# Performance work log

Hardware: AMD Instinct MI355X
Metric: run time of the kernel (lower is better)

## Reference

```python
import jax, jax.numpy as jnp
import numpy as np

B, N, H, NH, DEG, NREL = 4, 2048, 768, 12, 16, 64
HD = H // NH          # 64
E = B * N * DEG       # 131072 edges


def setup_inputs() -> dict:
    key = jax.random.key(0)
    ks = jax.random.split(key, 12)
    node_states = jax.random.normal(ks[0], (B, N, H), jnp.float32)

    # Structured edge list so every (batch, dst) pair has DEG distinct src
    # neighbors (unique+coalesce-stable, matching the coalesced sparse tensor).
    b = np.repeat(np.arange(B), N * DEG)
    dst = np.tile(np.repeat(np.arange(N), DEG), B)
    stride = N // DEG
    src = (dst + np.tile(np.arange(DEG), B * N) * stride) % N
    rel = np.random.default_rng(0).integers(0, NREL, size=E)
    edge_indices = jnp.asarray(np.stack([b, dst, src, rel]), jnp.int32)  # (4, E)

    s = 0.02
    Wq = s * jax.random.normal(ks[1], (H, H), jnp.float32)
    bq = s * jax.random.normal(ks[2], (H,), jnp.float32)
    Wk = s * jax.random.normal(ks[3], (H, H), jnp.float32)
    bk = s * jax.random.normal(ks[4], (H,), jnp.float32)
    Wv = s * jax.random.normal(ks[5], (H, H), jnp.float32)
    bv = s * jax.random.normal(ks[6], (H,), jnp.float32)
    # relation embedding tables; row 0 = TOKEN_TO_TOKEN_RELATION_ID zeroed
    Ek = (s * jax.random.normal(ks[7], (NREL, H), jnp.float32)).at[0].set(0.0)
    Ev = (s * jax.random.normal(ks[8], (NREL, H), jnp.float32)).at[0].set(0.0)
    return {"node_states": node_states, "edge_indices": edge_indices,
            "Wq": Wq, "bq": bq, "Wk": Wk, "bk": bk, "Wv": Wv, "bv": bv,
            "Ek": Ek, "Ev": Ev}


def reference(node_states, edge_indices, Wq, bq, Wk, bk, Wv, bv, Ek, Ev):
    Bsz, n_nodes, hidden = node_states.shape
    bi, dst, src, rel = edge_indices

    # dense projections (torch Linear: x @ W.T + b)
    Q = node_states @ Wq.T + bq
    K = node_states @ Wk.T + bk
    V = node_states @ Wv.T + bv

    def heads(x):  # (E, H) -> (E, NH, HD)
        return x.reshape(x.shape[0], NH, HD)

    Qe = heads(Q[bi, dst])     # query gathered at destination node
    Kn = heads(K[bi, src])     # key gathered at source node
    Vn = heads(V[bi, src])
    Ke = heads(Ek[rel])        # edge (relation) key embedding
    Ve = heads(Ev[rel])        # edge (relation) value embedding

    scale = jnp.sqrt(jnp.float32(HD))
    logits = (jnp.sum(Qe * Kn, -1) + jnp.sum(Qe * Ke, -1)) / scale  # (E, NH)

    # sparse softmax over src neighbors per (batch, dst) segment
    seg = bi * n_nodes + dst
    nseg = Bsz * n_nodes
    m = jax.ops.segment_max(logits, seg, num_segments=nseg)
    ex = jnp.exp(logits - m[seg])
    denom = jax.ops.segment_sum(ex, seg, num_segments=nseg)
    attn = ex / denom[seg]                                           # (E, NH)

    # weighted scatter-sum of (node value + edge value) back to dst nodes
    out_e = (attn[..., None] * (Vn + Ve)).reshape(-1, hidden)        # (E, H)
    out = jax.ops.segment_sum(out_e, seg, num_segments=nseg)
    return out.reshape(Bsz, n_nodes, hidden)
```

## Files before the change

kernel.cpp:

```cpp
#include <hip/hip_runtime.h>
#include <hip/hip_bf16.h>

#define BSZ 4
#define NN 2048
#define HH 768
#define NOUT 2304
#define NHEAD 12
#define HD 64
#define DEG 16
#define NREL 64
#define MTOT (BSZ * NN)
#define ETOT (MTOT * DEG)
#define QPAD 776

typedef __attribute__((ext_vector_type(4))) float f32x4;
typedef __attribute__((ext_vector_type(8))) short bf16x8;

__device__ __forceinline__ unsigned short f2bf(float f) {
    union { float f; unsigned int u; } v; v.f = f;
    unsigned int r = v.u + 0x7FFFu + ((v.u >> 16) & 1u);
    return (unsigned short)(r >> 16);
}
__device__ __forceinline__ float bf2f(unsigned short u) {
    union { unsigned int u; float f; } v; v.u = ((unsigned int)u) << 16;
    return v.f;
}

__device__ __forceinline__ void gload16(const unsigned short* g, unsigned short* l) {
    __builtin_amdgcn_global_load_lds(
        (const __attribute__((address_space(1))) unsigned int*)g,
        (__attribute__((address_space(3))) unsigned int*)l,
        16, 0, 0);
}

__global__ __launch_bounds__(256) void convert_all(
    const float* __restrict__ X,
    const float* __restrict__ Wq, const float* __restrict__ Wk,
    const float* __restrict__ Wv,
    const float* __restrict__ bq, const float* __restrict__ bk,
    const float* __restrict__ bv,
    const float* __restrict__ Ek, const float* __restrict__ Ev,
    unsigned short* __restrict__ Xb, unsigned short* __restrict__ Wb,
    float* __restrict__ biasb,
    unsigned short* __restrict__ Ekb, unsigned short* __restrict__ Evb)
{
    const int blk = blockIdx.x;
    if (blk < 3072) {
        const size_t i = ((size_t)blk * 256 + threadIdx.x) * 8;
        const float4 a = *(const float4*)(X + i);
        const float4 b = *(const float4*)(X + i + 4);
        bf16x8 o;
        o[0] = f2bf(a.x); o[1] = f2bf(a.y); o[2] = f2bf(a.z); o[3] = f2bf(a.w);
        o[4] = f2bf(b.x); o[5] = f2bf(b.y); o[6] = f2bf(b.z); o[7] = f2bf(b.w);
        *(bf16x8*)(Xb + i) = o;
    } else if (blk < 3936) {
        const int tid = (blk - 3072) * 256 + threadIdx.x;
        const size_t i = (size_t)tid * 8;
        const int row = (int)(i / HH);
        const size_t off = i - (size_t)row * HH;
        const float* src = (row < HH) ? (Wq + (size_t)row * HH)
                         : (row < 2 * HH) ? (Wk + (size_t)(row - HH) * HH)
                                          : (Wv + (size_t)(row - 2 * HH) * HH);
        const float4 a = *(const float4*)(src + off);
        const float4 b = *(const float4*)(src + off + 4);
        bf16x8 o;
        o[0] = f2bf(a.x); o[1] = f2bf(a.y); o[2] = f2bf(a.z); o[3] = f2bf(a.w);
        o[4] = f2bf(b.x); o[5] = f2bf(b.y); o[6] = f2bf(b.z); o[7] = f2bf(b.w);
        *(bf16x8*)(Wb + i) = o;
        if (tid < NOUT) {
            biasb[tid] = (tid < HH) ? bq[tid]
                       : (tid < 2 * HH) ? bk[tid - HH] : bv[tid - 2 * HH];
        }
    } else {
        const int blk2 = blk - 3936;
        const int h2 = blk2 / 24;
        const int b2 = blk2 % 24;
        const float* src = h2 ? Ev : Ek;
        unsigned short* dst = h2 ? Evb : Ekb;
        const size_t i = ((size_t)b2 * 256 + threadIdx.x) * 8;
        const float4 a = *(const float4*)(src + i);
        const float4 b = *(const float4*)(src + i + 4);
        bf16x8 o;
        o[0] = f2bf(a.x); o[1] = f2bf(a.y); o[2] = f2bf(a.z); o[3] = f2bf(a.w);
        o[4] = f2bf(b.x); o[5] = f2bf(b.y); o[6] = f2bf(b.z); o[7] = f2bf(b.w);
        *(bf16x8*)(dst + i) = o;
    }
}

__global__ __launch_bounds__(512) void qkv_mfma(
    const unsigned short* __restrict__ Xb,
    const unsigned short* __restrict__ Wb,
    const float* __restrict__ biasb,
    unsigned short* __restrict__ Qb,
    unsigned short* __restrict__ Kb, unsigned short* __restrict__ Vb)
{
    __shared__ unsigned short As0[256 * 32], As1[256 * 32];
    __shared__ unsigned short Bs0[128 * 32], Bs1[128 * 32];

    const int t    = threadIdx.x;
    const int lane = t & 63;
    const int w    = t >> 6;
    const int wr   = w >> 1;
    const int wc   = w & 1;

    const int bid = blockIdx.y * 18 + blockIdx.x;
    const int swz = (bid & 7) * 72 + (bid >> 3);
    const int bn  = (swz % 18) * 128;
    const int bm  = (swz / 18) * 256;

    const int srow  = w * 16 + (lane >> 2);
    const int sslot = ((lane & 3) ^ ((lane >> 2) & 3)) * 8;

    const unsigned short* Asrc0 = Xb + (size_t)(bm + srow) * HH + sslot;
    const unsigned short* Asrc1 = Xb + (size_t)(bm + 128 + srow) * HH + sslot;
    const unsigned short* Bsrc  = Wb + (size_t)(bn + srow) * HH + sslot;

    const int dstoff0 = w * 64 * 8;
    const int dstoff1 = (512 + w * 64) * 8;

    f32x4 acc[4][4];
    #pragma unroll
    for (int ni = 0; ni < 4; ++ni)
        #pragma unroll
        for (int mi = 0; mi < 4; ++mi)
            acc[ni][mi] = (f32x4){0.f, 0.f, 0.f, 0.f};

    const int fr  = lane & 15;
    const int fkp = (((lane >> 4) ^ (lane & 3))) * 8;

#define STAGE(AS, BS, K0) do {                 \
    gload16(Asrc0 + (K0), (AS) + dstoff0);     \
    gload16(Asrc1 + (K0), (AS) + dstoff1);     \
    gload16(Bsrc  + (K0), (BS) + dstoff0);     \
} while (0)

#define COMPUTE(AS, BS) do {                                                  \
    bf16x8 a_[4], b_[4];                                                      \
    _Pragma("unroll")                                                         \
    for (int mi = 0; mi < 4; ++mi)                                            \
        a_[mi] = *(const bf16x8*)((AS) + (wr * 64 + mi * 16 + fr) * 32 + fkp);\
    _Pragma("unroll")                                                         \
    for (int ni = 0; ni < 4; ++ni)                                            \
        b_[ni] = *(const bf16x8*)((BS) + (wc * 64 + ni * 16 + fr) * 32 + fkp);\
    _Pragma("unroll")                                                         \
    for (int ni = 0; ni < 4; ++ni)                                            \
        _Pragma("unroll")                                                     \
        for (int mi = 0; mi < 4; ++mi)                                        \
            acc[ni][mi] = __builtin_amdgcn_mfma_f32_16x16x32_bf16(            \
                b_[ni], a_[mi], acc[ni][mi], 0, 0, 0);                        \
} while (0)

#define WAITV3  asm volatile("s_waitcnt vmcnt(3)" ::: "memory")
#define WAITV0  asm volatile("s_waitcnt vmcnt(0)" ::: "memory")
#define BAR     do { __builtin_amdgcn_s_barrier();                  \
                     asm volatile("" ::: "memory"); } while (0)

    STAGE(As0, Bs0, 0);
    STAGE(As1, Bs1, 32);

    for (int kt = 0; kt < 22; kt += 2) {
        WAITV3; BAR;
        COMPUTE(As0, Bs0);
        BAR;
        STAGE(As0, Bs0, (kt + 2) * 32);
        WAITV3; BAR;
        COMPUTE(As1, Bs1);
        BAR;
        STAGE(As1, Bs1, (kt + 3) * 32);
    }
    WAITV3; BAR;
    COMPUTE(As0, Bs0);
    WAITV0; BAR;
    COMPUTE(As1, Bs1);
#undef STAGE
#undef COMPUTE
#undef WAITV3
#undef WAITV0
#undef BAR

    const int cm = lane & 15;
    const int cn = (lane >> 4) * 4;

    unsigned short* outb; int ncol0;
    if (bn < HH)          { outb = Qb; ncol0 = bn; }
    else if (bn < 2 * HH) { outb = Kb; ncol0 = bn - HH; }
    else                  { outb = Vb; ncol0 = bn - 2 * HH; }

    #pragma unroll
    for (int ni = 0; ni < 4; ++ni) {
        const int nloc = wc * 64 + ni * 16 + cn;
        const float4 b4 = *(const float4*)(biasb + bn + nloc);
        #pragma unroll
        for (int mi = 0; mi < 4; ++mi) {
            const int grow = bm + wr * 64 + mi * 16 + cm;
            ushort4 o;
            o.x = f2bf(acc[ni][mi][0] + b4.x);
            o.y = f2bf(acc[ni][mi][1] + b4.y);
            o.z = f2bf(acc[ni][mi][2] + b4.z);
            o.w = f2bf(acc[ni][mi][3] + b4.w);
            *(ushort4*)(outb + (size_t)grow * HH + ncol0 + nloc) = o;
        }
    }
}

__global__ __launch_bounds__(256) void s2_kernel(
    const unsigned short* __restrict__ Qb,
    const unsigned short* __restrict__ Ekb,
    unsigned short* __restrict__ S2b)
{
    const int t    = threadIdx.x;
    const int lane = t & 63;
    const int w    = t >> 6;
    const int h    = blockIdx.y;
    const int m0   = blockIdx.x * 64 + w * 16;

    const int fr  = lane & 15;
    const int fk8 = (lane >> 4) * 8;

    bf16x8 a[2];
    #pragma unroll
    for (int kk = 0; kk < 2; ++kk)
        a[kk] = *(const bf16x8*)(Qb + (size_t)(m0 + fr) * HH + h * HD + kk * 32 + fk8);

    #pragma unroll
    for (int rt = 0; rt < 4; ++rt) {
        f32x4 acc = (f32x4){0.f, 0.f, 0.f, 0.f};
        #pragma unroll
        for (int kk = 0; kk < 2; ++kk) {
            const bf16x8 bfr = *(const bf16x8*)(
                Ekb + (size_t)(rt * 16 + fr) * HH + h * HD + kk * 32 + fk8);
            acc = __builtin_amdgcn_mfma_f32_16x16x32_bf16(bfr, a[kk], acc, 0, 0, 0);
        }
        const int m   = m0 + (lane & 15);
        const int rel = rt * 16 + (lane >> 4) * 4;
        ushort4 o;
        o.x = f2bf(acc[0]); o.y = f2bf(acc[1]);
        o.z = f2bf(acc[2]); o.w = f2bf(acc[3]);
        *(ushort4*)(S2b + (size_t)m * HH + h * HD + rel) = o;
    }
}

__global__ __launch_bounds__(512) void attn_class(
    const unsigned short* __restrict__ Qb, const unsigned short* __restrict__ Kb,
    const unsigned short* __restrict__ Vb,
    const unsigned short* __restrict__ S2b, const unsigned short* __restrict__ Evb,
    const int* __restrict__ eidx, float* __restrict__ out)
{
    const int bc = blockIdx.x;
    const int b  = bc >> 7;
    const int r  = bc & 127;
    const int t  = threadIdx.x;
    const int lane = t & 63;
    const int w    = t >> 6;

    __shared__ unsigned short s_V[16][QPAD];
    __shared__ float s_attn[16][NHEAD][16];
    __shared__ int s_relslot[16][16];

    if (t < 256) {
        const int j = t >> 4, d = t & 15;
        const size_t e = ((size_t)(b * NN + r + j * 128)) * DEG + d;
        const int src = eidx[2 * ETOT + e];
        const int rel = eidx[3 * ETOT + e];
        const int slot = ((src - r) >> 7) & 15;
        s_relslot[j][slot] = rel;
    }
    for (int g = t; g < 1536; g += 512) {
        const int row = g / 96;
        const int off = (g - row * 96) * 8;
        *(bf16x8*)&s_V[row][off] =
            *(const bf16x8*)(Vb + (size_t)(b * NN + r + row * 128) * HH + off);
    }
    __syncthreads();

    {
        const int fr  = lane & 15;
        const int ig  = lane >> 4;
        const int fk8 = ig * 8;
        const size_t rowb = (size_t)(b * NN + r + fr * 128) * HH;
        #pragma unroll
        for (int hh = 0; hh < 2; ++hh) {
            if (hh == 1 && w >= 4) continue;
            const int h = (hh == 0) ? w : 8 + w;
            f32x4 acc = (f32x4){0.f, 0.f, 0.f, 0.f};
            #pragma unroll
            for (int kk = 0; kk < 2; ++kk) {
                const bf16x8 qf = *(const bf16x8*)(Qb + rowb + h * HD + kk * 32 + fk8);
                const bf16x8 kf = *(const bf16x8*)(Kb + rowb + h * HD + kk * 32 + fk8);
                acc = __builtin_amdgcn_mfma_f32_16x16x32_bf16(kf, qf, acc, 0, 0, 0);
            }
            float p[4];
            #pragma unroll
            for (int rr = 0; rr < 4; ++rr) {
                const int rel = s_relslot[fr][ig * 4 + rr];
                p[rr] = (acc[rr] + bf2f(S2b[rowb + h * HD + rel])) * 0.125f;
            }
            float mx = fmaxf(fmaxf(p[0], p[1]), fmaxf(p[2], p[3]));
            mx = fmaxf(mx, __shfl_xor(mx, 16, 64));
            mx = fmaxf(mx, __shfl_xor(mx, 32, 64));
            float sum = 0.f;
            #pragma unroll
            for (int rr = 0; rr < 4; ++rr) { p[rr] = __expf(p[rr] - mx); sum += p[rr]; }
            sum += __shfl_xor(sum, 16, 64);
            sum += __shfl_xor(sum, 32, 64);
            const float inv = 1.0f / sum;
            f32x4 pa = (f32x4){p[0] * inv, p[1] * inv, p[2] * inv, p[3] * inv};
            *(f32x4*)&s_attn[fr][h][ig * 4] = pa;
        }
    }
    __syncthreads();

    {
        const int j = t >> 5;
        const int c = t & 31;
        const int col0 = c * 24;
        float acc[24];
        #pragma unroll
        for (int u = 0; u < 24; ++u) acc[u] = 0.f;

        #pragma unroll
        for (int i = 0; i < 16; ++i) {
            const unsigned short* evrow = Evb + (size_t)s_relslot[j][i] * HH + col0;
            #pragma unroll
            for (int u = 0; u < 6; ++u) {
                const int col = col0 + u * 4;
                const float wgt = s_attn[j][col >> 6][i];
                const ushort4 v4 = *(const ushort4*)&s_V[i][col];
                const ushort4 e4 = *(const ushort4*)(evrow + u * 4);
                acc[u * 4 + 0] += wgt * (bf2f(v4.x) + bf2f(e4.x));
                acc[u * 4 + 1] += wgt * (bf2f(v4.y) + bf2f(e4.y));
                acc[u * 4 + 2] += wgt * (bf2f(v4.z) + bf2f(e4.z));
                acc[u * 4 + 3] += wgt * (bf2f(v4.w) + bf2f(e4.w));
            }
        }
        float* orow = out + (size_t)(b * NN + r + j * 128) * HH + col0;
        #pragma unroll
        for (int u = 0; u < 6; ++u)
            *(f32x4*)(orow + u * 4) = (f32x4){acc[u*4], acc[u*4+1], acc[u*4+2], acc[u*4+3]};
    }
}

extern "C" void kernel_launch(void* const* d_in, const int* in_sizes, int n_in,
                              void* d_out, int out_size, void* d_ws, size_t ws_size,
                              hipStream_t stream)
{
    const float* X  = (const float*)d_in[0];
    const int* eidx = (const int*)d_in[1];
    const float* Wq = (const float*)d_in[2];
    const float* bq = (const float*)d_in[3];
    const float* Wk = (const float*)d_in[4];
    const float* bk = (const float*)d_in[5];
    const float* Wv = (const float*)d_in[6];
    const float* bv = (const float*)d_in[7];
    const float* Ek = (const float*)d_in[8];
    const float* Ev = (const float*)d_in[9];
    float* out = (float*)d_out;

    char* ws = (char*)d_ws;
    unsigned short* Qb  = (unsigned short*)ws;
    unsigned short* Kb  = (unsigned short*)(ws + 12582912);
    unsigned short* Vb  = (unsigned short*)(ws + 25165824);
    unsigned short* Xb  = (unsigned short*)(ws + 37748736);
    unsigned short* Wb  = (unsigned short*)(ws + 50331648);
    float* biasb        = (float*)(ws + 53870592);
    unsigned short* S2b = (unsigned short*)(ws + 53879808);
    unsigned short* Ekb = (unsigned short*)(ws + 66462720);
    unsigned short* Evb = (unsigned short*)(ws + 66561024);

    convert_all<<<3984, 256, 0, stream>>>(X, Wq, Wk, Wv, bq, bk, bv, Ek, Ev,
                                          Xb, Wb, biasb, Ekb, Evb);

    dim3 g(NOUT / 128, MTOT / 256);
    qkv_mfma<<<g, 512, 0, stream>>>(Xb, Wb, biasb, Qb, Kb, Vb);

    s2_kernel<<<dim3(128, NHEAD), 256, 0, stream>>>(Qb, Ekb, S2b);

    attn_class<<<BSZ * 128, 512, 0, stream>>>(Qb, Kb, Vb, S2b, Evb, eidx, out);
}
```

Before: 102.2 us.

## Split attention blocks into four column quarters and prefetch V into registers

The attention kernel now launches four blocks per 16-node class. Each block handles a 192-column quarter, which is three heads, and runs 256 threads. V tiles are loaded into registers before the softmax and written to shared memory afterwards, so the global loads overlap the MFMA/softmax work. This gives 2048 smaller blocks instead of 512, spreading the work over more CUs, at the cost of the edge-index/relation setup being repeated in every quarter block.

```diff
diff --git a/kernel.cpp b/kernel.cpp
--- a/kernel.cpp
+++ b/kernel.cpp
@@ -11,7 +11,6 @@
 #define NREL 64
 #define MTOT (BSZ * NN)
 #define ETOT (MTOT * DEG)
-#define QPAD 776
 
 typedef __attribute__((ext_vector_type(4))) float f32x4;
 typedef __attribute__((ext_vector_type(8))) short bf16x8;
@@ -240,24 +239,26 @@
     }
 }
 
-__global__ __launch_bounds__(512) void attn_class(
+__global__ __launch_bounds__(256) void attn_class(
     const unsigned short* __restrict__ Qb, const unsigned short* __restrict__ Kb,
     const unsigned short* __restrict__ Vb,
     const unsigned short* __restrict__ S2b, const unsigned short* __restrict__ Evb,
     const int* __restrict__ eidx, float* __restrict__ out)
 {
-    const int bc = blockIdx.x;
-    const int b  = bc >> 7;
-    const int r  = bc & 127;
-    const int t  = threadIdx.x;
+    const int blk = blockIdx.x;
+    const int q   = blk & 3;
+    const int bc  = blk >> 2;
+    const int b   = bc >> 7;
+    const int r   = bc & 127;
+    const int t   = threadIdx.x;
     const int lane = t & 63;
     const int w    = t >> 6;
 
-    __shared__ unsigned short s_V[16][QPAD];
-    __shared__ float s_attn[16][NHEAD][16];
+    __shared__ unsigned short s_V[16][200];
+    __shared__ float s_attn[16][3][16];
     __shared__ int s_relslot[16][16];
 
-    if (t < 256) {
+    {
         const int j = t >> 4, d = t & 15;
         const size_t e = ((size_t)(b * NN + r + j * 128)) * DEG + d;
         const int src = eidx[2 * ETOT + e];
@@ -265,65 +266,71 @@
         const int slot = ((src - r) >> 7) & 15;
         s_relslot[j][slot] = rel;
     }
-    for (int g = t; g < 1536; g += 512) {
-        const int row = g / 96;
-        const int off = (g - row * 96) * 8;
-        *(bf16x8*)&s_V[row][off] =
-            *(const bf16x8*)(Vb + (size_t)(b * NN + r + row * 128) * HH + off);
+
+    ushort4 vreg[3];
+    int vrow[3], vcol[3];
+    #pragma unroll
+    for (int u = 0; u < 3; ++u) {
+        const int g   = t + u * 256;
+        const int row = g / 48;
+        const int col = (g - row * 48) * 4;
+        vrow[u] = row; vcol[u] = col;
+        vreg[u] = *(const ushort4*)(
+            Vb + (size_t)(b * NN + r + row * 128) * HH + q * 192 + col);
     }
     __syncthreads();
 
-    {
+    if (w < 3) {
+        const int h   = q * 3 + w;
         const int fr  = lane & 15;
         const int ig  = lane >> 4;
         const int fk8 = ig * 8;
         const size_t rowb = (size_t)(b * NN + r + fr * 128) * HH;
-        #pragma unroll
-        for (int hh = 0; hh < 2; ++hh) {
-            if (hh == 1 && w >= 4) continue;
-            const int h = (hh == 0) ? w : 8 + w;
-            f32x4 acc = (f32x4){0.f, 0.f, 0.f, 0.f};
+        f32x4 acc = (f32x4){0.f, 0.f, 0.f, 0.f};
+        #pragma unroll
+        for (int kk = 0; kk < 2; ++kk) {
+            const bf16x8 qf = *(const bf16x8*)(Qb + rowb + h * HD + kk * 32 + fk8);
+            const bf16x8 kf = *(const bf16x8*)(Kb + rowb + h * HD + kk * 32 + fk8);
+            acc = __builtin_amdgcn_mfma_f32_16x16x32_bf16(kf, qf, acc, 0, 0, 0);
+        }
+        float p[4];
+        #pragma unroll
+        for (int rr = 0; rr < 4; ++rr) {
+            const int rel = s_relslot[fr][ig * 4 + rr];
+            p[rr] = (acc[rr] + bf2f(S2b[rowb + h * HD + rel])) * 0.125f;
+        }
+        float mx = fmaxf(fmaxf(p[0], p[1]), fmaxf(p[2], p[3]));
+        mx = fmaxf(mx, __shfl_xor(mx, 16, 64));
+        mx = fmaxf(mx, __shfl_xor(mx, 32, 64));
+        float sum = 0.f;
+        #pragma unroll
+        for (int rr = 0; rr < 4; ++rr) { p[rr] = __expf(p[rr] - mx); sum += p[rr]; }
+        sum += __shfl_xor(sum, 16, 64);
+        sum += __shfl_xor(sum, 32, 64);
+        const float inv = 1.0f / sum;
+        f32x4 pa = (f32x4){p[0] * inv, p[1] * inv, p[2] * inv, p[3] * inv};
+        *(f32x4*)&s_attn[fr][w][ig * 4] = pa;
+    }
+
+    #pragma unroll
+    for (int u = 0; u < 3; ++u)
+        *(ushort4*)&s_V[vrow[u]][vcol[u]] = vreg[u];
+    __syncthreads();
+
+    {
+        const int j  = t >> 4;
+        const int ct = t & 15;
+        float acc[12];
+        #pragma unroll
+        for (int u = 0; u < 12; ++u) acc[u] = 0.f;
+
+        #pragma unroll
+        for (int i = 0; i < 16; ++i) {
+            const unsigned short* evrow =
+                Evb + (size_t)s_relslot[j][i] * HH + q * 192 + ct * 12;
             #pragma unroll
-            for (int kk = 0; kk < 2; ++kk) {
-                const bf16x8 qf = *(const bf16x8*)(Qb + rowb + h * HD + kk * 32 + fk8);
-                const bf16x8 kf = *(const bf16x8*)(Kb + rowb + h * HD + kk * 32 + fk8);
-                acc = __builtin_amdgcn_mfma_f32_16x16x32_bf16(kf, qf, acc, 0, 0, 0);
-            }
-            float p[4];
-            #pragma unroll
-            for (int rr = 0; rr < 4; ++rr) {
-                const int rel = s_relslot[fr][ig * 4 + rr];
-                p[rr] = (acc[rr] + bf2f(S2b[rowb + h * HD + rel])) * 0.125f;
-            }
-            float mx = fmaxf(fmaxf(p[0], p[1]), fmaxf(p[2], p[3]));
-            mx = fmaxf(mx, __shfl_xor(mx, 16, 64));
-            mx = fmaxf(mx, __shfl_xor(mx, 32, 64));
-            float sum = 0.f;
-            #pragma unroll
-            for (int rr = 0; rr < 4; ++rr) { p[rr] = __expf(p[rr] - mx); sum += p[rr]; }
-            sum += __shfl_xor(sum, 16, 64);
-            sum += __shfl_xor(sum, 32, 64);
-            const float inv = 1.0f / sum;
-            f32x4 pa = (f32x4){p[0] * inv, p[1] * inv, p[2] * inv, p[3] * inv};
-            *(f32x4*)&s_attn[fr][h][ig * 4] = pa;
-        }
-    }
-    __syncthreads();
-
-    {
-        const int j = t >> 5;
-        const int c = t & 31;
-        const int col0 = c * 24;
-        float acc[24];
-        #pragma unroll
-        for (int u = 0; u < 24; ++u) acc[u] = 0.f;
-
-        #pragma unroll
-        for (int i = 0; i < 16; ++i) {
-            const unsigned short* evrow = Evb + (size_t)s_relslot[j][i] * HH + col0;
-            #pragma unroll
-            for (int u = 0; u < 6; ++u) {
-                const int col = col0 + u * 4;
+            for (int u = 0; u < 3; ++u) {
+                const int col = ct * 12 + u * 4;
                 const float wgt = s_attn[j][col >> 6][i];
                 const ushort4 v4 = *(const ushort4*)&s_V[i][col];
                 const ushort4 e4 = *(const ushort4*)(evrow + u * 4);
@@ -333,10 +340,11 @@
                 acc[u * 4 + 3] += wgt * (bf2f(v4.w) + bf2f(e4.w));
             }
         }
-        float* orow = out + (size_t)(b * NN + r + j * 128) * HH + col0;
-        #pragma unroll
-        for (int u = 0; u < 6; ++u)
-            *(f32x4*)(orow + u * 4) = (f32x4){acc[u*4], acc[u*4+1], acc[u*4+2], acc[u*4+3]};
+        float* orow = out + (size_t)(b * NN + r + j * 128) * HH + q * 192 + ct * 12;
+        #pragma unroll
+        for (int u = 0; u < 3; ++u)
+            *(f32x4*)(orow + u * 4) =
+                (f32x4){acc[u*4], acc[u*4+1], acc[u*4+2], acc[u*4+3]};
     }
 }
 
@@ -375,5 +383,5 @@
 
     s2_kernel<<<dim3(128, NHEAD), 256, 0, stream>>>(Qb, Ekb, S2b);
 
-    attn_class<<<BSZ * 128, 512, 0, stream>>>(Qb, Kb, Vb, S2b, Evb, eidx, out);
-}
+    attn_class<<<BSZ * 128 * 4, 256, 0, stream>>>(Qb, Kb, Vb, S2b, Evb, eidx, out);
+}
```

Result: faster. 95.38 us (-6.7%).
